# Kernel optimization log

Hardware: AMD Instinct MI355X
Metric: run time of the kernel (lower is better)

Reference implementation:

```python
import jax, jax.numpy as jnp
import numpy as np

K = 4096
CIN = 256


def _kaiming_uniform(key, shape):
    # torch kaiming_uniform_ default: gain=sqrt(2), bound = gain*sqrt(3/fan_in)
    fan_in = shape[1]
    bound = np.sqrt(6.0 / fan_in)
    return jax.random.uniform(key, shape, jnp.float32, -bound, bound)


def _linear_weight(key, shape):
    # torch nn.Linear default init: U(-1/sqrt(fan_in), 1/sqrt(fan_in))
    bound = 1.0 / np.sqrt(shape[1])
    return jax.random.uniform(key, shape, jnp.float32, -bound, bound)


def setup_inputs() -> dict:
    key = jax.random.key(0)
    k0, k1, k2, k3, k4 = jax.random.split(key, 5)
    latent = jax.random.normal(k0, (16, CIN, 32, 32), jnp.float32)
    temperature = jnp.float32(1.0)
    codebook = _kaiming_uniform(k1, (K, CIN))
    wq = _linear_weight(k2, (CIN, CIN))
    wk = _linear_weight(k3, (CIN, CIN))
    wv = _linear_weight(k4, (CIN, CIN))
    return {"latent": latent, "temperature": temperature, "codebook": codebook,
            "wq": wq, "wk": wk, "wv": wv}


def reference(latent, temperature, codebook, wq, wk, wv):
    # deterministic=True, additionWeight=True, dropout=None
    cin = latent.shape[1]
    scale = jnp.sqrt(jnp.asarray(cin, latent.dtype))
    q = jnp.einsum('nchw,dc->nhwd', latent, wq)      # [n,h,w,cin], Linear: x @ W^T
    kmat = codebook @ wk.T                           # [k,cin]
    v = codebook @ wv.T                              # [k,cin]
    logit = jnp.einsum('nhwc,kc->nhwk', q, kmat) / scale
    soft = jax.nn.softmax(logit, axis=-1)
    idx = jnp.argmax(logit, axis=-1)                 # [n,h,w]
    soft_v = jnp.einsum('nhwk,kc->nhwc', soft, v)
    hard_v = v[idx]                                  # one-hot @ v == gather
    result = jax.lax.stop_gradient(hard_v - soft_v) + soft_v
    quantized = jnp.transpose(result, (0, 3, 1, 2))  # [n,cin,h,w]
    return (quantized, idx.astype(jnp.uint8), logit, v)
```

## Files before the change

### kernel.cpp

```cpp
#include <hip/hip_runtime.h>
#include <math.h>
#include <float.h>

#define CIN 256
#define KCB 4096
#define NPOS 16384

#define OFF_QUANT 0
#define OFF_IDX   4194304
#define OFF_LOGIT 4210688
#define OFF_V     71319552

#define MARGIN 5e-4f

typedef short bf16x8 __attribute__((ext_vector_type(8)));
typedef float f32x4 __attribute__((ext_vector_type(4)));

__device__ __forceinline__ unsigned short rne_bf16(float x) {
  const unsigned u = __float_as_uint(x);
  return (unsigned short)((u + 0x7FFFu + ((u >> 16) & 1u)) >> 16);
}

__device__ __forceinline__ void gload_lds16(const void* g, void* l) {
  __builtin_amdgcn_global_load_lds(
      (const __attribute__((address_space(1))) unsigned int*)g,
      (__attribute__((address_space(3))) unsigned int*)l, 16, 0, 0);
}

__device__ __forceinline__ void top2_merge(float& m1, int& i1, float& m2,
                                           float om1, int oi1, float om2) {
  if (om1 > m1 || (om1 == m1 && oi1 < i1)) {
    m2 = fmaxf(m1, om2);
    m1 = om1;
    i1 = oi1;
  } else {
    m2 = fmaxf(m2, fmaxf(om1, om2));
  }
}

__global__ __launch_bounds__(256) void kvq_kernel(
    const float* __restrict__ cb, const float* __restrict__ wk,
    const float* __restrict__ wv, const float* __restrict__ latent,
    const float* __restrict__ wq, unsigned short* __restrict__ kb,
    float* __restrict__ kf, float* __restrict__ vout,
    unsigned short* __restrict__ qb, float* __restrict__ qf) {
  __shared__ float sh[16][CIN];
  const int t = threadIdx.x;
  if (blockIdx.x < 256) {
    const int k0 = blockIdx.x * 16;
#pragma unroll
    for (int i = 0; i < 16; ++i)
      sh[i][t] = cb[(size_t)(k0 + i) * CIN + t];
    __syncthreads();
    float acck[16], accv[16];
#pragma unroll
    for (int r = 0; r < 16; ++r) { acck[r] = 0.f; accv[r] = 0.f; }
    const float* wkr = wk + (size_t)t * CIN;
    const float* wvr = wv + (size_t)t * CIN;
    for (int j = 0; j < CIN; ++j) {
      const float a = wkr[j];
      const float b = wvr[j];
#pragma unroll
      for (int r = 0; r < 16; ++r) {
        const float c = sh[r][j];
        acck[r] = fmaf(c, a, acck[r]);
        accv[r] = fmaf(c, b, accv[r]);
      }
    }
#pragma unroll
    for (int r = 0; r < 16; ++r) {
      const float xk = acck[r];
      kb[(size_t)(k0 + r) * CIN + t] = rne_bf16(xk);
      kf[(size_t)(k0 + r) * CIN + t] = xk;
      vout[(size_t)(k0 + r) * CIN + t] = accv[r];
    }
  } else {
    const int p0 = (blockIdx.x - 256) * 16;
    const int n = p0 >> 10, hw0 = p0 & 1023;
    const float* lbase =
        latent + (size_t)n * (CIN * 1024) + (size_t)t * 1024 + hw0;
#pragma unroll
    for (int i4 = 0; i4 < 4; ++i4) {
      float4 v4 = *(const float4*)(lbase + i4 * 4);
      sh[i4 * 4 + 0][t] = v4.x;
      sh[i4 * 4 + 1][t] = v4.y;
      sh[i4 * 4 + 2][t] = v4.z;
      sh[i4 * 4 + 3][t] = v4.w;
    }
    __syncthreads();
    float acc[16];
#pragma unroll
    for (int r = 0; r < 16; ++r) acc[r] = 0.f;
    const float* wqr = wq + (size_t)t * CIN;
    for (int j = 0; j < CIN; ++j) {
      const float w = wqr[j];
#pragma unroll
      for (int r = 0; r < 16; ++r) acc[r] = fmaf(sh[r][j], w, acc[r]);
    }
#pragma unroll
    for (int r = 0; r < 16; ++r) {
      qb[(size_t)(p0 + r) * CIN + t] = rne_bf16(acc[r]);
      qf[(size_t)(p0 + r) * CIN + t] = acc[r];
    }
  }
}

__global__ __launch_bounds__(256, 4) void logit_kernel(
    const unsigned short* __restrict__ qb, const unsigned short* __restrict__ kb,
    float* __restrict__ logit, float* __restrict__ pm1,
    int* __restrict__ pi1, float* __restrict__ pm2) {
  __shared__ __align__(16) unsigned short smem[2][2][128 * 32];

  const int t = threadIdx.x;
  const int b = blockIdx.x;
  const int x = (b & 7) * 512 + (b >> 3);
  const int bn = x & 31, bm = x >> 5;
  const int n0 = bn * 128, m0 = bm * 128;

  const int lane = t & 63, w = t >> 6;
  const int wr = w >> 1, wc = w & 1;
  const int fr = lane & 15, fq = lane >> 4;

  const int srow = t >> 2;
  const int spc = t & 3;
  const int slog = spc ^ ((srow >> 1) & 3);
  const int sldse = srow * 32 + spc * 8;

  int aoff[4], boff[4];
#pragma unroll
  for (int mi = 0; mi < 4; ++mi) {
    const int ar = wr * 64 + mi * 16 + fr;
    aoff[mi] = ar * 32 + (fq ^ ((ar >> 1) & 3)) * 8;
  }
#pragma unroll
  for (int ni = 0; ni < 4; ++ni) {
    const int br = wc * 64 + ni * 16 + fr;
    boff[ni] = br * 32 + (fq ^ ((br >> 1) & 3)) * 8;
  }

  f32x4 acc[4][4];
#pragma unroll
  for (int i = 0; i < 4; ++i)
#pragma unroll
    for (int j = 0; j < 4; ++j) acc[i][j] = (f32x4)(0.f);

#pragma unroll
  for (int h = 0; h < 2; ++h) {
    const int r = h * 64 + srow;
    gload_lds16(qb + (size_t)(m0 + r) * CIN + slog * 8,
                &smem[0][0][h * 2048 + sldse]);
    gload_lds16(kb + (size_t)(n0 + r) * CIN + slog * 8,
                &smem[0][1][h * 2048 + sldse]);
  }
  asm volatile("s_waitcnt vmcnt(0)" ::: "memory");
  __syncthreads();

  for (int s = 0; s < 8; ++s) {
    const int buf = s & 1;
    if (s < 7) {
      const int k0 = (s + 1) * 32;
      const int nb = buf ^ 1;
#pragma unroll
      for (int h = 0; h < 2; ++h) {
        const int r = h * 64 + srow;
        gload_lds16(qb + (size_t)(m0 + r) * CIN + k0 + slog * 8,
                    &smem[nb][0][h * 2048 + sldse]);
        gload_lds16(kb + (size_t)(n0 + r) * CIN + k0 + slog * 8,
                    &smem[nb][1][h * 2048 + sldse]);
      }
    }
    bf16x8 a[4], bfr[4];
#pragma unroll
    for (int mi = 0; mi < 4; ++mi) a[mi] = *(const bf16x8*)&smem[buf][0][aoff[mi]];
#pragma unroll
    for (int ni = 0; ni < 4; ++ni) bfr[ni] = *(const bf16x8*)&smem[buf][1][boff[ni]];
#pragma unroll
    for (int mi = 0; mi < 4; ++mi)
#pragma unroll
      for (int ni = 0; ni < 4; ++ni)
        acc[mi][ni] = __builtin_amdgcn_mfma_f32_16x16x32_bf16(
            a[mi], bfr[ni], acc[mi][ni], 0, 0, 0);
    asm volatile("s_waitcnt vmcnt(0)" ::: "memory");
    __syncthreads();
  }

  const float sc = 0.0625f;
  float* S1 = (float*)&smem[0][0][0];
  unsigned* S2 = (unsigned*)((char*)&smem[0][0][0] + 16384);
#pragma unroll
  for (int mi = 0; mi < 4; ++mi)
#pragma unroll
    for (int i = 0; i < 4; ++i) {
      const int rt = wr * 64 + mi * 16 + fq * 4 + i;
      const int row = m0 + rt;
      float vals[4];
#pragma unroll
      for (int ni = 0; ni < 4; ++ni) {
        vals[ni] = acc[mi][ni][i] * sc;
        __builtin_nontemporal_store(
            vals[ni], &logit[(size_t)row * KCB + n0 + wc * 64 + ni * 16 + fr]);
      }
      float m1 = vals[0], m2 = -FLT_MAX;
      int ni1 = 0;
#pragma unroll
      for (int ni = 1; ni < 4; ++ni) {
        if (vals[ni] > m1) { m2 = m1; m1 = vals[ni]; ni1 = ni; }
        else if (vals[ni] > m2) m2 = vals[ni];
      }
      const int sb = (wc * 128 + rt) * 16 + fr;
      S1[sb] = m1;
      S2[sb] = (__float_as_uint(m2) & ~3u) | (unsigned)ni1;
    }
  __syncthreads();
  if (t < 128) {
    float m1 = -FLT_MAX, m2 = -FLT_MAX;
    int i1 = 0;
#pragma unroll
    for (int wc2 = 0; wc2 < 2; ++wc2)
#pragma unroll
      for (int f4 = 0; f4 < 4; ++f4) {
        const int base = (wc2 * 128 + t) * 16 + f4 * 4;
        const float4 am1 = *(const float4*)&S1[base];
        const uint4 au2 = *(const uint4*)&S2[base];
        const unsigned ue[4] = {au2.x, au2.y, au2.z, au2.w};
        const float me[4] = {am1.x, am1.y, am1.z, am1.w};
#pragma unroll
        for (int e = 0; e < 4; ++e) {
          const int col = wc2 * 64 + (int)(ue[e] & 3u) * 16 + f4 * 4 + e;
          top2_merge(m1, i1, m2, me[e], col, __uint_as_float(ue[e] & ~3u));
        }
      }
    pm1[(size_t)(m0 + t) * 32 + bn] = m1;
    pi1[(size_t)(m0 + t) * 32 + bn] = n0 + i1;
    pm2[(size_t)(m0 + t) * 32 + bn] = m2;
  }
}

__global__ __launch_bounds__(256) void easyrefine_kernel(
    const float* __restrict__ pm1, const int* __restrict__ pi1,
    const float* __restrict__ pm2, const float* __restrict__ logit,
    const float* __restrict__ qf, const float* __restrict__ kf,
    int* __restrict__ rowidx_ws) {
  __shared__ float s_rowmax[16];
  __shared__ int s_flag[16];
  __shared__ int s_nflag;
  __shared__ int s_cnt[4];
  __shared__ int s_list[4][64];

  const int t = threadIdx.x;
  const int p0 = blockIdx.x * 16;
  if (t == 0) s_nflag = 0;
  __syncthreads();

  {
    const int r = t >> 4, l16 = t & 15;
    const int p = p0 + r;
    const size_t base = (size_t)p * 32;
    float m1 = pm1[base + l16], m2 = pm2[base + l16];
    int i1 = pi1[base + l16];
    top2_merge(m1, i1, m2, pm1[base + 16 + l16], pi1[base + 16 + l16],
               pm2[base + 16 + l16]);
#pragma unroll
    for (int mask = 1; mask < 16; mask <<= 1) {
      const float om1 = __shfl_xor(m1, mask, 64);
      const int oi1 = __shfl_xor(i1, mask, 64);
      const float om2 = __shfl_xor(m2, mask, 64);
      top2_merge(m1, i1, m2, om1, oi1, om2);
    }
    if (l16 == 0) {
      rowidx_ws[p] = i1;
      s_rowmax[r] = m1;
      if (m1 - m2 <= MARGIN) {
        const int pos = atomicAdd(&s_nflag, 1);
        s_flag[pos] = r;
      }
    }
  }
  __syncthreads();

  const int w = t >> 6, lane = t & 63;
  const int nf = s_nflag;
  for (int fi = w; fi < nf; fi += 4) {
    const int p = p0 + s_flag[fi];
    const float4 qv = *(const float4*)&qf[(size_t)p * CIN + lane * 4];
    if (lane == 0) s_cnt[w] = 0;
    const float thr = s_rowmax[s_flag[fi]] - MARGIN;
    const float* lrow = logit + (size_t)p * KCB;
    for (int it = 0; it < 16; ++it) {
      const float4 xv = *(const float4*)&lrow[lane * 4 + it * 256];
      const float xe[4] = {xv.x, xv.y, xv.z, xv.w};
#pragma unroll
      for (int e = 0; e < 4; ++e) {
        if (xe[e] > thr) {
          const int pos = atomicAdd(&s_cnt[w], 1);
          if (pos < 64) s_list[w][pos] = lane * 4 + it * 256 + e;
        }
      }
    }
    const int nc = min(s_cnt[w], 64);
    float bestv = -FLT_MAX;
    int bestj = 0x7fffffff;
    for (int ci = 0; ci < nc; ++ci) {
      const int j = s_list[w][ci];
      const float4 kv4 = *(const float4*)&kf[(size_t)j * CIN + lane * 4];
      float d = qv.x * kv4.x + qv.y * kv4.y + qv.z * kv4.z + qv.w * kv4.w;
#pragma unroll
      for (int m = 1; m < 64; m <<= 1) d += __shfl_xor(d, m, 64);
      const float val = d * 0.0625f;
      if (val > bestv || (val == bestv && j < bestj)) { bestv = val; bestj = j; }
    }
    if (lane == 0) rowidx_ws[p] = bestj;
  }
}

__global__ __launch_bounds__(256) void gather_kernel(
    const int* __restrict__ rowidx_ws, const float* __restrict__ vout,
    float* __restrict__ outq, float* __restrict__ outidx) {
  __shared__ int rowidx[16];
  const int t = threadIdx.x;
  const int p0 = blockIdx.x * 16;
  if (t < 16) rowidx[t] = rowidx_ws[p0 + t];
  __syncthreads();
  const int n = p0 >> 10, hw0 = p0 & 1023;
  float res[16];
#pragma unroll
  for (int r2 = 0; r2 < 16; ++r2)
    res[r2] = vout[(size_t)rowidx[r2] * CIN + t];
  float* ob = outq + (size_t)n * (CIN * 1024) + (size_t)t * 1024 + hw0;
#pragma unroll
  for (int i4 = 0; i4 < 4; ++i4)
    *(float4*)&ob[i4 * 4] = make_float4(res[i4 * 4 + 0], res[i4 * 4 + 1],
                                        res[i4 * 4 + 2], res[i4 * 4 + 3]);
  if (t < 16) outidx[p0 + t] = (float)(rowidx[t] & 255);
}

extern "C" void kernel_launch(void* const* d_in, const int* in_sizes, int n_in,
                              void* d_out, int out_size, void* d_ws,
                              size_t ws_size, hipStream_t stream) {
  const float* latent = (const float*)d_in[0];
  const float* codebook = (const float*)d_in[2];
  const float* wq = (const float*)d_in[3];
  const float* wk = (const float*)d_in[4];
  const float* wv = (const float*)d_in[5];

  float* out = (float*)d_out;
  float* outq = out + OFF_QUANT;
  float* outidx = out + OFF_IDX;
  float* outlogit = out + OFF_LOGIT;
  float* outv = out + OFF_V;

  float* qf = outq;

  char* ws = (char*)d_ws;
  unsigned short* qb = (unsigned short*)(ws + 0);
  unsigned short* kb = (unsigned short*)(ws + 8388608);
  float* kf = (float*)(ws + 10485760);
  float* pm1 = (float*)(ws + 14680064);
  int* pi1 = (int*)(ws + 16777216);
  float* pm2 = (float*)(ws + 18874368);
  int* rowidx_ws = (int*)(ws + 20971520);

  kvq_kernel<<<256 + NPOS / 16, 256, 0, stream>>>(codebook, wk, wv, latent, wq,
                                                  kb, kf, outv, qb, qf);
  logit_kernel<<<4096, 256, 0, stream>>>(qb, kb, outlogit, pm1, pi1, pm2);
  easyrefine_kernel<<<NPOS / 16, 256, 0, stream>>>(pm1, pi1, pm2, outlogit, qf,
                                                   kf, rowidx_ws);
  gather_kernel<<<NPOS / 16, 256, 0, stream>>>(rowidx_ws, outv, outq, outidx);
}
```

Baseline: 205.6 us.

## Triple-buffer LDS staging in logit GEMM with two-stage prefetch

Changes the logit kernel's global-to-LDS pipeline from double to triple buffering. It keeps two K-slices in flight and waits on vmcnt(4) instead of draining all loads each iteration. The aim is to hide global load latency behind MFMA work. In exchange, LDS use per block rises by half and the occupancy hint drops from 4 to 3 blocks per CU.

```diff
diff --git a/kernel.cpp b/kernel.cpp
--- a/kernel.cpp
+++ b/kernel.cpp
@@ -105,11 +105,11 @@
   }
 }
 
-__global__ __launch_bounds__(256, 4) void logit_kernel(
+__global__ __launch_bounds__(256, 3) void logit_kernel(
     const unsigned short* __restrict__ qb, const unsigned short* __restrict__ kb,
     float* __restrict__ logit, float* __restrict__ pm1,
     int* __restrict__ pi1, float* __restrict__ pm2) {
-  __shared__ __align__(16) unsigned short smem[2][2][128 * 32];
+  __shared__ __align__(16) unsigned short smem[3][2][128 * 32];
 
   const int t = threadIdx.x;
   const int b = blockIdx.x;
@@ -144,45 +144,53 @@
 #pragma unroll
     for (int j = 0; j < 4; ++j) acc[i][j] = (f32x4)(0.f);
 
-#pragma unroll
-  for (int h = 0; h < 2; ++h) {
-    const int r = h * 64 + srow;
-    gload_lds16(qb + (size_t)(m0 + r) * CIN + slog * 8,
-                &smem[0][0][h * 2048 + sldse]);
-    gload_lds16(kb + (size_t)(n0 + r) * CIN + slog * 8,
-                &smem[0][1][h * 2048 + sldse]);
-  }
-  asm volatile("s_waitcnt vmcnt(0)" ::: "memory");
-  __syncthreads();
-
+#define STAGE(DST, K0)                                                       \
+  {                                                                          \
+    _Pragma("unroll") for (int h = 0; h < 2; ++h) {                          \
+      const int r = h * 64 + srow;                                           \
+      gload_lds16(qb + (size_t)(m0 + r) * CIN + (K0) + slog * 8,             \
+                  &smem[DST][0][h * 2048 + sldse]);                          \
+      gload_lds16(kb + (size_t)(n0 + r) * CIN + (K0) + slog * 8,             \
+                  &smem[DST][1][h * 2048 + sldse]);                          \
+    }                                                                        \
+  }
+
+  STAGE(0, 0)
+  STAGE(1, 32)
+  asm volatile("s_waitcnt vmcnt(4)" ::: "memory");
+  __syncthreads();
+
+#pragma unroll
   for (int s = 0; s < 8; ++s) {
-    const int buf = s & 1;
-    if (s < 7) {
-      const int k0 = (s + 1) * 32;
-      const int nb = buf ^ 1;
-#pragma unroll
-      for (int h = 0; h < 2; ++h) {
-        const int r = h * 64 + srow;
-        gload_lds16(qb + (size_t)(m0 + r) * CIN + k0 + slog * 8,
-                    &smem[nb][0][h * 2048 + sldse]);
-        gload_lds16(kb + (size_t)(n0 + r) * CIN + k0 + slog * 8,
-                    &smem[nb][1][h * 2048 + sldse]);
-      }
+    const int bufc = s % 3;
+    if (s < 6) {
+      const int nb = (s + 2) % 3;
+      STAGE(nb, (s + 2) * 32)
     }
     bf16x8 a[4], bfr[4];
 #pragma unroll
-    for (int mi = 0; mi < 4; ++mi) a[mi] = *(const bf16x8*)&smem[buf][0][aoff[mi]];
-#pragma unroll
-    for (int ni = 0; ni < 4; ++ni) bfr[ni] = *(const bf16x8*)&smem[buf][1][boff[ni]];
+    for (int mi = 0; mi < 4; ++mi)
+      a[mi] = *(const bf16x8*)&smem[bufc][0][aoff[mi]];
+#pragma unroll
+    for (int ni = 0; ni < 4; ++ni)
+      bfr[ni] = *(const bf16x8*)&smem[bufc][1][boff[ni]];
 #pragma unroll
     for (int mi = 0; mi < 4; ++mi)
 #pragma unroll
       for (int ni = 0; ni < 4; ++ni)
         acc[mi][ni] = __builtin_amdgcn_mfma_f32_16x16x32_bf16(
             a[mi], bfr[ni], acc[mi][ni], 0, 0, 0);
-    asm volatile("s_waitcnt vmcnt(0)" ::: "memory");
-    __syncthreads();
-  }
+    if (s < 6) {
+      asm volatile("s_waitcnt vmcnt(4)" ::: "memory");
+      __syncthreads();
+    } else if (s == 6) {
+      asm volatile("s_waitcnt vmcnt(0)" ::: "memory");
+      __syncthreads();
+    } else {
+      __syncthreads();
+    }
+  }
+#undef STAGE
 
   const float sc = 0.0625f;
   float* S1 = (float*)&smem[0][0][0];
```

Measured after the change: 222.4 us. 8.2% more time.
